# Optimization experiments

Measured on AMD Instinct MI355X. Metric: run time of the kernel, lower is better.

The kernel has to match this reference:

```python
import jax, jax.numpy as jnp
import numpy as np

D_MODEL = 1024
N_HEADS = 16
HEAD_DIM = D_MODEL // N_HEADS
WINDOW = 128
ROPE_BASE = 10000.0


def _rope_cos_sin(T, dim, dtype):
    inv_freq = 1.0 / (ROPE_BASE ** (jnp.arange(0, dim, 2, dtype=jnp.float32) / dim))
    freqs = jnp.arange(T, dtype=jnp.float32)[:, None] * inv_freq[None, :]  # [T, dim/2]
    emb = jnp.concatenate([freqs, freqs], axis=-1)  # [T, dim]
    return jnp.cos(emb).astype(dtype), jnp.sin(emb).astype(dtype)


def _rotate_half(x):
    h = x.shape[-1] // 2
    return jnp.concatenate([-x[..., h:], x[..., :h]], axis=-1)


def _apply_rotary(x, cos, sin):
    # x: [B, T, H, Dh]; cos/sin: [T, Dh]
    c = cos[None, :, None, :]
    s = sin[None, :, None, :]
    return x * c + _rotate_half(x) * s


def setup_inputs() -> dict:
    key = jax.random.key(0)
    ks = jax.random.split(key, 6)
    B, T = 2, 2048
    query = jax.random.normal(ks[0], (B, T, D_MODEL), dtype=jnp.float32)
    scale = 1.0 / np.sqrt(D_MODEL)
    Wq = jax.random.normal(ks[1], (D_MODEL, D_MODEL), dtype=jnp.float32) * scale
    Wk = jax.random.normal(ks[2], (D_MODEL, D_MODEL), dtype=jnp.float32) * scale
    Wv = jax.random.normal(ks[3], (D_MODEL, D_MODEL), dtype=jnp.float32) * scale
    Wo = jax.random.normal(ks[4], (D_MODEL, D_MODEL), dtype=jnp.float32) * scale
    bo = jax.random.normal(ks[5], (D_MODEL,), dtype=jnp.float32) * 0.01
    return {"query": query, "Wq": Wq, "Wk": Wk, "Wv": Wv, "Wo": Wo, "bo": bo}


def reference(query, Wq, Wk, Wv, Wo, bo):
    # Sliding-window causal self-attention with rotary embeddings (eval mode, no dropout).
    B, T, D = query.shape
    H, Dh = N_HEADS, HEAD_DIM
    sm_scale = Dh ** -0.5

    # Projections (torch nn.Linear: y = x @ W.T)
    q = (query @ Wq.T).reshape(B, T, H, Dh)
    k = (query @ Wk.T).reshape(B, T, H, Dh)
    v = (query @ Wv.T).reshape(B, T, H, Dh)

    cos, sin = _rope_cos_sin(T, Dh, query.dtype)
    q = _apply_rotary(q, cos, sin)
    k = _apply_rotary(k, cos, sin)

    # [B, H, T, Dh]
    q = q.transpose(0, 2, 1, 3)
    k = k.transpose(0, 2, 1, 3)
    v = v.transpose(0, 2, 1, 3)

    scores = jnp.einsum('bhqd,bhkd->bhqk', q, k) * sm_scale

    # Causal sliding-window mask: masked if j > i or j < i - (WINDOW - 1)
    i = jnp.arange(T)[:, None]
    j = jnp.arange(T)[None, :]
    mask = (j > i) | (j < i - (WINDOW - 1))  # [T, T], True = masked
    scores = jnp.where(mask[None, None], jnp.float32(-jnp.inf), scores)

    attn = jax.nn.softmax(scores, axis=-1)
    out = jnp.einsum('bhqk,bhkd->bhqd', attn, v)  # [B, H, T, Dh]
    out = out.transpose(0, 2, 1, 3).reshape(B, T, D)
    return out @ Wo.T + bo
```

## Files before the change

kernel.cpp:

```cpp
#include <hip/hip_runtime.h>

#define BATCH 2
#define SEQ   2048
#define DMODEL 1024
#define NHEADS 16
#define HDIM   64
#define WINDOW 128
#define ROWS  (BATCH * SEQ)

typedef __bf16 bf16x8 __attribute__((ext_vector_type(8)));
typedef __bf16 bf16x4 __attribute__((ext_vector_type(4)));
typedef float  f32x4  __attribute__((ext_vector_type(4)));

__device__ __forceinline__ void async_load16(const __bf16* g, __bf16* l) {
    __builtin_amdgcn_global_load_lds(
        (const __attribute__((address_space(1))) unsigned int*)g,
        (__attribute__((address_space(3))) unsigned int*)l, 16, 0, 0);
}

__global__ __launch_bounds__(256) void convert_bf16(
    const float* __restrict__ X,
    const float* __restrict__ Wq, const float* __restrict__ Wk,
    const float* __restrict__ Wv, const float* __restrict__ Wo,
    __bf16* __restrict__ Xbf, __bf16* __restrict__ Wbf,
    float* __restrict__ ct, float* __restrict__ st)
{
    const int XN8 = ROWS * DMODEL / 8;
    const int WN8 = DMODEL * DMODEL / 8;
    const int TOT = XN8 + 4 * WN8;
    int idx = blockIdx.x * blockDim.x + threadIdx.x;

    if (idx < TOT) {
        const float* src;
        __bf16* dst;
        if (idx < XN8) {
            src = X + (size_t)idx * 8;
            dst = Xbf + (size_t)idx * 8;
        } else {
            int rel = idx - XN8;
            int w = rel >> 17;
            int off = rel & (WN8 - 1);
            const float* Wp = (w == 0) ? Wq : (w == 1) ? Wk : (w == 2) ? Wv : Wo;
            src = Wp + (size_t)off * 8;
            dst = Wbf + (size_t)rel * 8;
        }
        float4 a = *(const float4*)src;
        float4 b = *(const float4*)(src + 4);
        bf16x8 o;
        o[0] = (__bf16)a.x; o[1] = (__bf16)a.y; o[2] = (__bf16)a.z; o[3] = (__bf16)a.w;
        o[4] = (__bf16)b.x; o[5] = (__bf16)b.y; o[6] = (__bf16)b.z; o[7] = (__bf16)b.w;
        *(bf16x8*)dst = o;
    } else if (idx < TOT + SEQ * 32) {
        int k = idx - TOT;
        int t = k >> 5, d = k & 31;
        float ang = (float)t * expf(-(float)d * 0.28782313662425572f);
        float s, c;
        sincosf(ang, &s, &c);
        ct[k] = c; st[k] = s;
    }
}

template<int TM, int TN>
__device__ __forceinline__ void gemm_mfma_body(
    const __bf16* __restrict__ A, const __bf16* __restrict__ B,
    void* __restrict__ Cout, const float* __restrict__ bias,
    const float* __restrict__ ct, const float* __restrict__ st,
    int mode, int N, int K, int m0, int n0)
{
    constexpr bool SQ = (TN == 128);
    constexpr int NI = SQ ? 4 : (TM / 64);
    constexpr int NAC = TM / 64;
    constexpr int NBC = TN / 64;
    __shared__ __bf16 As[4][TM * 32];
    __shared__ __bf16 Bs[4][TN * 32];

    const int tid  = threadIdx.x;
    const int lane = tid & 63;
    const int wv   = tid >> 6;
    const int wrow = SQ ? (wv >> 1) * 64 : wv * (TM / 4);
    const int wcol = SQ ? (wv & 1) * 64 : 0;

    const int srow = lane >> 2;
    const int schk = (lane & 3) ^ ((lane >> 3) & 3);
    const int arbase = wv * (TM / 4);
    const int brbase = wv * (TN / 4);

    const __bf16* gA0 = A + (size_t)(m0 + arbase + srow) * K + 8 * schk;
    const __bf16* gA1 = gA0 + (size_t)16 * K;
    const __bf16* gB0 = B + (size_t)(n0 + brbase + srow) * K + 8 * schk;
    const __bf16* gB1 = gB0 + (size_t)16 * K;

    const int frow = lane & 15;
    const int fsw  = 8 * ((lane >> 4) ^ ((frow >> 1) & 3));

    f32x4 acc[NI][4];
#pragma unroll
    for (int i = 0; i < NI; ++i)
#pragma unroll
        for (int j = 0; j < 4; ++j) {
            acc[i][j][0] = 0.f; acc[i][j][1] = 0.f;
            acc[i][j][2] = 0.f; acc[i][j][3] = 0.f;
        }

    for (int k0 = 0; k0 < K; k0 += 128) {
        __syncthreads();
#pragma unroll
        for (int h = 0; h < 4; ++h) {
            async_load16(gA0 + k0 + 32 * h, As[h] + arbase * 32);
            if (NAC == 2)
                async_load16(gA1 + k0 + 32 * h, As[h] + (arbase + 16) * 32);
            async_load16(gB0 + k0 + 32 * h, Bs[h] + brbase * 32);
            if (NBC == 2)
                async_load16(gB1 + k0 + 32 * h, Bs[h] + (brbase + 16) * 32);
        }
        __syncthreads();

#pragma unroll
        for (int h = 0; h < 4; ++h) {
            bf16x8 afr[NI], bfr[4];
#pragma unroll
            for (int i = 0; i < NI; ++i)
                afr[i] = *(const bf16x8*)(As[h] + (wrow + 16 * i + frow) * 32 + fsw);
#pragma unroll
            for (int j = 0; j < 4; ++j)
                bfr[j] = *(const bf16x8*)(Bs[h] + (wcol + 16 * j + frow) * 32 + fsw);
#pragma unroll
            for (int i = 0; i < NI; ++i)
#pragma unroll
                for (int j = 0; j < 4; ++j)
                    acc[i][j] = __builtin_amdgcn_mfma_f32_16x16x32_bf16(
                        afr[i], bfr[j], acc[i][j], 0, 0, 0);
        }
    }

#pragma unroll
    for (int i = 0; i < NI; ++i) {
#pragma unroll
        for (int r = 0; r < 4; ++r) {
            int row = m0 + wrow + i * 16 + (lane >> 4) * 4 + r;
            if (mode <= 1) {
                int t = row & (SEQ - 1);
#pragma unroll
                for (int j = 0; j < 2; ++j) {
                    int dd = j * 16 + (lane & 15);
                    float c = ct[t * 32 + dd];
                    float s = st[t * 32 + dd];
                    float v0 = acc[i][j][r], v1 = acc[i][j + 2][r];
                    float n0v = v0 * c - v1 * s;
                    float n1v = v1 * c + v0 * s;
                    if (mode == 0) { n0v *= 0.125f; n1v *= 0.125f; }
                    acc[i][j][r] = n0v; acc[i][j + 2][r] = n1v;
                }
            }
#pragma unroll
            for (int j = 0; j < 4; ++j) {
                int col = n0 + wcol + j * 16 + (lane & 15);
                float v = acc[i][j][r];
                if (mode == 3)
                    ((float*)Cout)[(size_t)row * N + col] = v + bias[col];
                else
                    ((__bf16*)Cout)[(size_t)row * N + col] = (__bf16)v;
            }
        }
    }
}

template<int GX, int GY>
__device__ __forceinline__ void xcd_swizzle(int& xb, int& yb)
{
    int id = blockIdx.x + GX * blockIdx.y;
    int q  = id & 7;
    int s  = id >> 3;
    xb = s % GX;
    yb = (GY / 8) * q + s / GX;
}

__global__ __launch_bounds__(256) void gemm_qkv_bf(
    const __bf16* __restrict__ X, const __bf16* __restrict__ Wbf,
    __bf16* __restrict__ Qb, __bf16* __restrict__ Kb, __bf16* __restrict__ Vb,
    const float* __restrict__ ct, const float* __restrict__ st)
{
    const int z = blockIdx.z;
    const __bf16* W = Wbf + (size_t)z * (DMODEL * DMODEL);
    __bf16* C = (z == 0) ? Qb : (z == 1) ? Kb : Vb;
    int xb, yb;
    xcd_swizzle<8, 32>(xb, yb);
    gemm_mfma_body<128, 128>(X, W, C, nullptr, ct, st, z, DMODEL, DMODEL,
                             yb * 128, xb * 128);
}

__global__ __launch_bounds__(256) void gemm_out_bf(
    const __bf16* __restrict__ Abf, const __bf16* __restrict__ Wo,
    const float* __restrict__ bias, float* __restrict__ out)
{
    int xb, yb;
    xcd_swizzle<16, 64>(xb, yb);
    gemm_mfma_body<64, 64>(Abf, Wo, out, bias, nullptr, nullptr, 3,
                           DMODEL, DMODEL, yb * 64, xb * 64);
}

#define QTILE 64
#define KPAD  72
#define VPAD  200
#define PPAD  168

__global__ __launch_bounds__(256, 3) void attn_mfma(
    const __bf16* __restrict__ Qb, const __bf16* __restrict__ Kb,
    const __bf16* __restrict__ Vb, __bf16* __restrict__ Abf)
{
    __shared__ __bf16 KsPs[192 * KPAD];
    __shared__ __bf16 Vt[64 * VPAD];

    const int tid  = threadIdx.x;
    const int lane = tid & 63;
    const int wv   = tid >> 6;
    const int q0   = blockIdx.x * QTILE;
    const int h    = blockIdx.y;
    const int b    = blockIdx.z;
    const int jbase = q0 - 128;
    const size_t hoff = (size_t)h * HDIM;
    const int nloc  = lane & 15;
    const int mbase = (lane >> 4) * 4;
    const int fk    = (lane >> 4) * 8;

    const __bf16* Kg = Kb + (size_t)(b * SEQ) * DMODEL + hoff;
    const __bf16* Vg = Vb + (size_t)(b * SEQ) * DMODEL + hoff;

#pragma unroll
    for (int it = 0; it < 6; ++it) {
        int idx = tid + it * 256;
        int jt = idx >> 3;
        int dq = (idx & 7) * 8;
        int jg = jbase + jt;
        int jc = jg < 0 ? 0 : jg;
        bf16x8 kv = *(const bf16x8*)(Kg + (size_t)jc * DMODEL + dq);
        bf16x8 vv = *(const bf16x8*)(Vg + (size_t)jc * DMODEL + dq);
        *(bf16x8*)(KsPs + jt * KPAD + dq) = kv;
        const int jsw = jt ^ dq;
#pragma unroll
        for (int e = 0; e < 8; ++e) Vt[(dq + e) * VPAD + jsw] = vv[e];
    }
    __syncthreads();

    const __bf16* Qg = Qb + (size_t)(b * SEQ + q0 + 16 * wv + nloc) * DMODEL + hoff + fk;
    bf16x8 qfr0 = *(const bf16x8*)(Qg);
    bf16x8 qfr1 = *(const bf16x8*)(Qg + 32);

    f32x4 s[9];
    __builtin_amdgcn_s_setprio(1);
#pragma unroll
    for (int c = 0; c < 9; ++c) {
        const __bf16* kp = KsPs + (size_t)(16 * (wv + c) + nloc) * KPAD + fk;
        bf16x8 k0 = *(const bf16x8*)kp;
        bf16x8 k1 = *(const bf16x8*)(kp + 32);
        f32x4 z; z[0] = 0.f; z[1] = 0.f; z[2] = 0.f; z[3] = 0.f;
        z = __builtin_amdgcn_mfma_f32_16x16x32_bf16(qfr0, k0, z, 0, 0, 0);
        z = __builtin_amdgcn_mfma_f32_16x16x32_bf16(qfr1, k1, z, 0, 0, 0);
        s[c] = z;
    }
    __builtin_amdgcn_s_setprio(0);
    __syncthreads();

    float inv_row[4];
#pragma unroll
    for (int r = 0; r < 4; ++r) {
        int rl = 16 * wv + mbase + r;
        float mx = -INFINITY;
#pragma unroll
        for (int c = 0; c < 9; ++c) {
            int jt = 16 * (wv + c) + nloc;
            bool valid = (jt >= rl + 1) && (jt <= rl + 128) && (jbase + jt >= 0);
            float sv = valid ? s[c][r] : -INFINITY;
            s[c][r] = sv;
            mx = fmaxf(mx, sv);
        }
#pragma unroll
        for (int off = 8; off; off >>= 1) mx = fmaxf(mx, __shfl_xor(mx, off));
        float sum = 0.f;
#pragma unroll
        for (int c = 0; c < 9; ++c) {
            float p = __expf(s[c][r] - mx);
            s[c][r] = p;
            sum += p;
        }
#pragma unroll
        for (int off = 8; off; off >>= 1) sum += __shfl_xor(sum, off);
        inv_row[r] = 1.0f / sum;
    }

    __bf16* myP = KsPs + (size_t)wv * 16 * PPAD;
#pragma unroll
    for (int c = 0; c < 9; ++c)
#pragma unroll
        for (int r = 0; r < 4; ++r)
            myP[(mbase + r) * PPAD + 16 * c + nloc] = (__bf16)(s[c][r] * inv_row[r]);
#pragma unroll
    for (int r = 0; r < 4; ++r)
        myP[(mbase + r) * PPAD + 144 + nloc] = (__bf16)0.0f;

    asm volatile("" ::: "memory");
    __builtin_amdgcn_s_waitcnt(0);

    f32x4 o[4];
#pragma unroll
    for (int j = 0; j < 4; ++j) { o[j][0] = 0.f; o[j][1] = 0.f; o[j][2] = 0.f; o[j][3] = 0.f; }
    __builtin_amdgcn_s_setprio(1);
#pragma unroll
    for (int stp = 0; stp < 5; ++stp) {
        bf16x8 pf = *(const bf16x8*)(myP + nloc * PPAD + 32 * stp + fk);
        int vcol = 16 * wv + 32 * stp + fk;
        if (vcol >= 192) vcol = 0;
#pragma unroll
        for (int j = 0; j < 4; ++j) {
            int row = 16 * j + nloc;
            int vc  = vcol ^ (8 * ((2 * j + (nloc >> 3)) & 7));
            bf16x8 vf = *(const bf16x8*)(Vt + (size_t)row * VPAD + vc);
            o[j] = __builtin_amdgcn_mfma_f32_16x16x32_bf16(pf, vf, o[j], 0, 0, 0);
        }
    }
    __builtin_amdgcn_s_setprio(0);

    __bf16* Og = Abf + (size_t)(b * SEQ + q0 + 16 * wv) * DMODEL + hoff;
#pragma unroll
    for (int j = 0; j < 4; ++j)
#pragma unroll
        for (int r = 0; r < 4; ++r)
            Og[(size_t)(mbase + r) * DMODEL + 16 * j + nloc] = (__bf16)o[j][r];
}

extern "C" void kernel_launch(void* const* d_in, const int* in_sizes, int n_in,
                              void* d_out, int out_size, void* d_ws, size_t ws_size,
                              hipStream_t stream)
{
    const float* X  = (const float*)d_in[0];
    const float* Wq = (const float*)d_in[1];
    const float* Wk = (const float*)d_in[2];
    const float* Wv = (const float*)d_in[3];
    const float* Wo = (const float*)d_in[4];
    const float* bo = (const float*)d_in[5];
    float* out = (float*)d_out;

    const size_t MB = 1ull << 20;
    __bf16* Xbf = (__bf16*)d_ws;
    __bf16* Wbf = (__bf16*)((char*)d_ws + 8 * MB);
    __bf16* Qb  = (__bf16*)((char*)d_ws + 16 * MB);
    __bf16* Kb  = (__bf16*)((char*)d_ws + 24 * MB);
    __bf16* Vb  = (__bf16*)((char*)d_ws + 32 * MB);
    float*  ctab = (float*)((char*)d_ws + 40 * MB);
    float*  stab = (float*)((char*)d_ws + 41 * MB);
    __bf16* Abf = Xbf;

    {
        int total = (ROWS * DMODEL + 4 * DMODEL * DMODEL) / 8 + SEQ * 32;
        convert_bf16<<<(total + 255) / 256, 256, 0, stream>>>(
            X, Wq, Wk, Wv, Wo, Xbf, Wbf, ctab, stab);
    }
    {
        dim3 grid(DMODEL / 128, ROWS / 128, 3);
        gemm_qkv_bf<<<grid, 256, 0, stream>>>(Xbf, Wbf, Qb, Kb, Vb, ctab, stab);
    }
    {
        dim3 grid(SEQ / QTILE, NHEADS, BATCH);
        attn_mfma<<<grid, 256, 0, stream>>>(Qb, Kb, Vb, Abf);
    }
    {
        dim3 grid(DMODEL / 64, ROWS / 64, 1);
        gemm_out_bf<<<grid, 256, 0, stream>>>(Abf, Wbf + 3ull * DMODEL * DMODEL, bo, out);
    }
}
```

Measured before the change: 160.4 us.

## Split-K the output projection across two slices with atomic accumulation

The output projection GEMM is split along K into two halves launched as grid z, with each half atomically adding its partial result into the fp32 output (bias added by the first slice). The output buffer is zeroed inside the conversion kernel so the atomics have a clean target. This doubles the number of blocks for the out-projection to improve occupancy, at the cost of zeroing 16MB of output and issuing scalar fp32 atomics instead of plain stores.

```diff
diff --git a/kernel.cpp b/kernel.cpp
--- a/kernel.cpp
+++ b/kernel.cpp
@@ -23,11 +23,14 @@
     const float* __restrict__ Wq, const float* __restrict__ Wk,
     const float* __restrict__ Wv, const float* __restrict__ Wo,
     __bf16* __restrict__ Xbf, __bf16* __restrict__ Wbf,
-    float* __restrict__ ct, float* __restrict__ st)
+    float* __restrict__ ct, float* __restrict__ st,
+    float* __restrict__ outZ)
 {
     const int XN8 = ROWS * DMODEL / 8;
     const int WN8 = DMODEL * DMODEL / 8;
     const int TOT = XN8 + 4 * WN8;
+    const int RTE = TOT + SEQ * 32;
+    const int ZN8 = ROWS * DMODEL / 8;
     int idx = blockIdx.x * blockDim.x + threadIdx.x;
 
     if (idx < TOT) {
@@ -50,13 +53,18 @@
         o[0] = (__bf16)a.x; o[1] = (__bf16)a.y; o[2] = (__bf16)a.z; o[3] = (__bf16)a.w;
         o[4] = (__bf16)b.x; o[5] = (__bf16)b.y; o[6] = (__bf16)b.z; o[7] = (__bf16)b.w;
         *(bf16x8*)dst = o;
-    } else if (idx < TOT + SEQ * 32) {
+    } else if (idx < RTE) {
         int k = idx - TOT;
         int t = k >> 5, d = k & 31;
         float ang = (float)t * expf(-(float)d * 0.28782313662425572f);
         float s, c;
         sincosf(ang, &s, &c);
         ct[k] = c; st[k] = s;
+    } else if (idx < RTE + ZN8) {
+        int k = idx - RTE;
+        float4 z4; z4.x = 0.f; z4.y = 0.f; z4.z = 0.f; z4.w = 0.f;
+        *(float4*)(outZ + (size_t)k * 8)     = z4;
+        *(float4*)(outZ + (size_t)k * 8 + 4) = z4;
     }
 }
 
@@ -65,7 +73,7 @@
     const __bf16* __restrict__ A, const __bf16* __restrict__ B,
     void* __restrict__ Cout, const float* __restrict__ bias,
     const float* __restrict__ ct, const float* __restrict__ st,
-    int mode, int N, int K, int m0, int n0)
+    int mode, int N, int K, int LDA, int m0, int n0)
 {
     constexpr bool SQ = (TN == 128);
     constexpr int NI = SQ ? 4 : (TM / 64);
@@ -85,10 +93,10 @@
     const int arbase = wv * (TM / 4);
     const int brbase = wv * (TN / 4);
 
-    const __bf16* gA0 = A + (size_t)(m0 + arbase + srow) * K + 8 * schk;
-    const __bf16* gA1 = gA0 + (size_t)16 * K;
-    const __bf16* gB0 = B + (size_t)(n0 + brbase + srow) * K + 8 * schk;
-    const __bf16* gB1 = gB0 + (size_t)16 * K;
+    const __bf16* gA0 = A + (size_t)(m0 + arbase + srow) * LDA + 8 * schk;
+    const __bf16* gA1 = gA0 + (size_t)16 * LDA;
+    const __bf16* gB0 = B + (size_t)(n0 + brbase + srow) * LDA + 8 * schk;
+    const __bf16* gB1 = gB0 + (size_t)16 * LDA;
 
     const int frow = lane & 15;
     const int fsw  = 8 * ((lane >> 4) ^ ((frow >> 1) & 3));
@@ -158,6 +166,10 @@
                 float v = acc[i][j][r];
                 if (mode == 3)
                     ((float*)Cout)[(size_t)row * N + col] = v + bias[col];
+                else if (mode == 4)
+                    atomicAdd(&((float*)Cout)[(size_t)row * N + col], v + bias[col]);
+                else if (mode == 5)
+                    atomicAdd(&((float*)Cout)[(size_t)row * N + col], v);
                 else
                     ((__bf16*)Cout)[(size_t)row * N + col] = (__bf16)v;
             }
@@ -185,18 +197,21 @@
     __bf16* C = (z == 0) ? Qb : (z == 1) ? Kb : Vb;
     int xb, yb;
     xcd_swizzle<8, 32>(xb, yb);
-    gemm_mfma_body<128, 128>(X, W, C, nullptr, ct, st, z, DMODEL, DMODEL,
-                             yb * 128, xb * 128);
-}
-
-__global__ __launch_bounds__(256) void gemm_out_bf(
+    gemm_mfma_body<128, 128>(X, W, C, nullptr, ct, st, z, DMODEL,
+                             DMODEL, DMODEL, yb * 128, xb * 128);
+}
+
+__global__ __launch_bounds__(256) void gemm_out_split(
     const __bf16* __restrict__ Abf, const __bf16* __restrict__ Wo,
     const float* __restrict__ bias, float* __restrict__ out)
 {
     int xb, yb;
     xcd_swizzle<16, 64>(xb, yb);
-    gemm_mfma_body<64, 64>(Abf, Wo, out, bias, nullptr, nullptr, 3,
-                           DMODEL, DMODEL, yb * 64, xb * 64);
+    const int z = blockIdx.z;
+    const int koff = z * 512;
+    gemm_mfma_body<64, 64>(Abf + koff, Wo + koff, out, bias, nullptr, nullptr,
+                           z == 0 ? 4 : 5, DMODEL, 512, DMODEL,
+                           yb * 64, xb * 64);
 }
 
 #define QTILE 64
@@ -351,9 +366,10 @@
     __bf16* Abf = Xbf;
 
     {
-        int total = (ROWS * DMODEL + 4 * DMODEL * DMODEL) / 8 + SEQ * 32;
+        int total = (ROWS * DMODEL + 4 * DMODEL * DMODEL) / 8 + SEQ * 32
+                  + ROWS * DMODEL / 8;
         convert_bf16<<<(total + 255) / 256, 256, 0, stream>>>(
-            X, Wq, Wk, Wv, Wo, Xbf, Wbf, ctab, stab);
+            X, Wq, Wk, Wv, Wo, Xbf, Wbf, ctab, stab, out);
     }
     {
         dim3 grid(DMODEL / 128, ROWS / 128, 3);
@@ -364,7 +380,8 @@
         attn_mfma<<<grid, 256, 0, stream>>>(Qb, Kb, Vb, Abf);
     }
     {
-        dim3 grid(DMODEL / 64, ROWS / 64, 1);
-        gemm_out_bf<<<grid, 256, 0, stream>>>(Abf, Wbf + 3ull * DMODEL * DMODEL, bo, out);
-    }
-}
+        dim3 grid(DMODEL / 64, ROWS / 64, 2);
+        gemm_out_split<<<grid, 256, 0, stream>>>(
+            Abf, Wbf + 3ull * DMODEL * DMODEL, bo, out);
+    }
+}
```

New measurement: 187.9 us. 1.17x slower.
